# Kernel optimization log

Hardware: AMD Instinct MI355X
Metric: run time of the kernel (lower is better)

Reference implementation:

```python
import jax, jax.numpy as jnp
import numpy as np

N = 8192  # number of nodes


def _deg_norm(idx, n):
    # degree^{-1/2}, zero-degree clamped to 1 (DGL allow_zero_in_degree behavior)
    deg = jax.ops.segment_sum(jnp.ones(idx.shape[0], jnp.float32), idx, num_segments=n)
    return jax.lax.rsqrt(jnp.maximum(deg, 1.0))


def _graph_conv(h, src, dst, norm_src, norm_dst, W, b):
    # norm='both': scale at src, sparse sum-aggregate, scale at dst, then linear
    h = h * norm_src[:, None]
    m = jax.ops.segment_sum(h[src], dst, num_segments=h.shape[0])  # gather + scatter-add
    m = m * norm_dst[:, None]
    return m @ W + b


def setup_inputs() -> dict:
    key = jax.random.key(0)
    k = jax.random.split(key, 6)
    E = 262144
    x = jax.random.normal(k[0], (N, 256), jnp.float32)
    src = jax.random.randint(k[1], (E,), 0, N, jnp.int32)
    dst = jax.random.randint(k[2], (E,), 0, N, jnp.int32)
    W1 = jax.random.normal(k[3], (256, 128), jnp.float32) * (1.0 / np.sqrt(256))
    b1 = jnp.zeros((128,), jnp.float32)
    W2 = jax.random.normal(k[4], (128, 128), jnp.float32) * (1.0 / np.sqrt(128))
    b2 = jnp.zeros((128,), jnp.float32)
    return {"x": x, "src": src, "dst": dst, "W1": W1, "b1": b1, "W2": W2, "b2": b2}


def reference(x, src, dst, W1, b1, W2, b2):
    n = x.shape[0]
    norm_src = _deg_norm(src, n)  # out-degree norm
    norm_dst = _deg_norm(dst, n)  # in-degree norm
    # encode: GraphConv -> relu -> GraphConv  (dropout=0 -> identity)
    h = jax.nn.relu(_graph_conv(x, src, dst, norm_src, norm_dst, W1, b1))
    h = _graph_conv(h, src, dst, norm_src, norm_dst, W2, b2)
    # decode: sigmoid(h h^T), dense [N, N] reconstruction
    return jax.nn.sigmoid(h @ h.T)
```

## Files before the change

kernel.cpp:

```cpp
#include <hip/hip_runtime.h>
#include <hip/hip_bf16.h>

typedef __attribute__((ext_vector_type(8))) short short8;
typedef __attribute__((ext_vector_type(4))) float f32x4;

#define NNODES 8192
#define FDIM 128

__global__ void k_zero(int* __restrict__ p, int n) {
    int i = blockIdx.x * blockDim.x + threadIdx.x;
    if (i < n) p[i] = 0;
}

__global__ void k_deg_int(const int* __restrict__ src, const int* __restrict__ dst,
                          int* __restrict__ cnt_s, int* __restrict__ cnt_d, int E) {
    int e = blockIdx.x * blockDim.x + threadIdx.x;
    if (e < E) {
        atomicAdd(&cnt_s[src[e]], 1);
        atomicAdd(&cnt_d[dst[e]], 1);
    }
}

__global__ __launch_bounds__(256) void k_scan_norms(const int* __restrict__ cnt_s,
                                                    const int* __restrict__ cnt_d,
                                                    float* __restrict__ norm_s,
                                                    int* __restrict__ row_start,
                                                    int* __restrict__ cursor, int n) {
    __shared__ int partial[256];
    __shared__ int offs[257];
    int t = threadIdx.x;
    int base = t * 32;
#pragma unroll
    for (int i = 0; i < 32; ++i)
        norm_s[base + i] = rsqrtf(fmaxf((float)cnt_s[base + i], 1.0f));
    int local[32];
    int s = 0;
#pragma unroll
    for (int i = 0; i < 32; ++i) { local[i] = s; s += cnt_d[base + i]; }
    partial[t] = s;
    __syncthreads();
    if (t == 0) {
        int acc = 0;
        for (int i = 0; i < 256; ++i) { offs[i] = acc; acc += partial[i]; }
        offs[256] = acc;
    }
    __syncthreads();
    int o = offs[t];
#pragma unroll
    for (int i = 0; i < 32; ++i) {
        int v = o + local[i];
        row_start[base + i] = v;
        cursor[base + i] = v;
    }
    if (t == 0) row_start[n] = offs[256];
}

__global__ void k_fill(const int* __restrict__ src, const int* __restrict__ dst,
                       int* __restrict__ cursor, int* __restrict__ csr_src, int E) {
    int e = blockIdx.x * blockDim.x + threadIdx.x;
    if (e < E) {
        int pos = atomicAdd(&cursor[dst[e]], 1);
        csr_src[pos] = src[e];
    }
}

template<int K>
__global__ __launch_bounds__(256) void k_linear(const float* __restrict__ X,
                                                const float* __restrict__ W,
                                                const float* __restrict__ norm,
                                                float* __restrict__ Y) {
    __shared__ float xs[16][K];
    int t = threadIdx.x;
    int row0 = blockIdx.x * 16;
    constexpr int K4 = K / 4;
    constexpr int NCH = 16 * K4 / 256;
#pragma unroll
    for (int i = 0; i < NCH; ++i) {
        int c = t + i * 256;
        int r = c / K4, k4 = c % K4;
        *(float4*)&xs[r][k4 * 4] = *(const float4*)(X + (size_t)(row0 + r) * K + k4 * 4);
    }
    __syncthreads();

    int lane = t & 31, g = t >> 5;
    int r0 = g * 2, r1 = g * 2 + 1;
    int c = lane * 4;
    f32x4 acc0 = {0.f, 0.f, 0.f, 0.f}, acc1 = {0.f, 0.f, 0.f, 0.f};
    for (int k = 0; k < K; k += 4) {
        f32x4 x0 = *(f32x4*)&xs[r0][k];
        f32x4 x1 = *(f32x4*)&xs[r1][k];
#pragma unroll
        for (int kk = 0; kk < 4; ++kk) {
            f32x4 w = *(const f32x4*)(W + (size_t)(k + kk) * FDIM + c);
            acc0 += w * x0[kk];
            acc1 += w * x1[kk];
        }
    }
    float n0 = norm[row0 + r0], n1 = norm[row0 + r1];
    *(f32x4*)(Y + (size_t)(row0 + r0) * FDIM + c) = acc0 * n0;
    *(f32x4*)(Y + (size_t)(row0 + r1) * FDIM + c) = acc1 * n1;
}

static __device__ inline unsigned short f2bf(float f) {
    union { float f; unsigned int u; } a; a.f = f;
    unsigned int u = a.u;
    unsigned int r = u + 0x7FFFu + ((u >> 16) & 1u);
    return (unsigned short)(r >> 16);
}

template<int MODE>
__global__ __launch_bounds__(256) void k_gather_agg(const float* __restrict__ Y,
                                                    const int* __restrict__ row_start,
                                                    const int* __restrict__ csr_src,
                                                    const float* __restrict__ bias,
                                                    void* __restrict__ outp) {
    int t = threadIdx.x;
    int node = blockIdx.x * 8 + (t >> 5);
    int c4 = (t & 31) << 2;
    int beg = row_start[node], end = row_start[node + 1];
    f32x4 acc0 = {0.f, 0.f, 0.f, 0.f}, acc1 = {0.f, 0.f, 0.f, 0.f};
    int e = beg;
    for (; e + 3 < end; e += 4) {
        int s0 = csr_src[e], s1 = csr_src[e + 1], s2 = csr_src[e + 2], s3 = csr_src[e + 3];
        f32x4 v0 = *(const f32x4*)(Y + ((size_t)s0 << 7) + c4);
        f32x4 v1 = *(const f32x4*)(Y + ((size_t)s1 << 7) + c4);
        f32x4 v2 = *(const f32x4*)(Y + ((size_t)s2 << 7) + c4);
        f32x4 v3 = *(const f32x4*)(Y + ((size_t)s3 << 7) + c4);
        acc0 += v0; acc1 += v1; acc0 += v2; acc1 += v3;
    }
    for (; e < end; ++e) {
        int s0 = csr_src[e];
        acc0 += *(const f32x4*)(Y + ((size_t)s0 << 7) + c4);
    }
    f32x4 acc = acc0 + acc1;
    float scale = rsqrtf(fmaxf((float)(end - beg), 1.0f));
    f32x4 b = *(const f32x4*)(bias + c4);
    f32x4 v = acc * scale + b;
    if (MODE == 0) {
#pragma unroll
        for (int i = 0; i < 4; ++i) v[i] = fmaxf(v[i], 0.f);
        *(f32x4*)((float*)outp + ((size_t)node << 7) + c4) = v;
    } else {
        ushort4 u;
        u.x = f2bf(v[0]); u.y = f2bf(v[1]); u.z = f2bf(v[2]); u.w = f2bf(v[3]);
        *(ushort4*)((unsigned short*)outp + ((size_t)node << 7) + c4) = u;
    }
}

__global__ __launch_bounds__(256) void k_decode(const __hip_bfloat16* __restrict__ H,
                                                float* __restrict__ C) {
    const int ti = blockIdx.x, tj = blockIdx.y;
    if (tj < ti) return;
    __shared__ __align__(16) unsigned char smem[65536];
    unsigned char* sA = smem;
    unsigned char* sB = smem + 32768;
    const int t = threadIdx.x;
    const unsigned char* gH = (const unsigned char*)H;

#pragma unroll
    for (int i = 0; i < 8; ++i) {
        int chunk = t + i * 256;
        int row = chunk >> 4;
        int cc = (chunk & 15) << 4;
        int lofs = row * 256 + (cc ^ ((row & 7) << 4));
        *(float4*)(sA + lofs) = *(const float4*)(gH + ((size_t)(ti * 128 + row) << 8) + cc);
        *(float4*)(sB + lofs) = *(const float4*)(gH + ((size_t)(tj * 128 + row) << 8) + cc);
    }
    __syncthreads();

    const int w = t >> 6, lane = t & 63;
    const int wr = (w >> 1) * 64, wc = (w & 1) * 64;
    const int lr = lane & 15;
    const int lk = (lane >> 4) * 16;

    f32x4 acc[4][4] = {};

#pragma unroll
    for (int ks = 0; ks < 4; ++ks) {
        short8 af[4], bfr[4];
#pragma unroll
        for (int mi = 0; mi < 4; ++mi) {
            int row = wr + mi * 16 + lr;
            int off = row * 256 + ((ks * 64 + lk) ^ ((row & 7) << 4));
            af[mi] = *(const short8*)(sA + off);
        }
#pragma unroll
        for (int ni = 0; ni < 4; ++ni) {
            int row = wc + ni * 16 + lr;
            int off = row * 256 + ((ks * 64 + lk) ^ ((row & 7) << 4));
            bfr[ni] = *(const short8*)(sB + off);
        }
#pragma unroll
        for (int mi = 0; mi < 4; ++mi)
#pragma unroll
            for (int ni = 0; ni < 4; ++ni)
                acc[mi][ni] = __builtin_amdgcn_mfma_f32_16x16x32_bf16(af[mi], bfr[ni],
                                                                      acc[mi][ni], 0, 0, 0);
    }

    const int rbase = (lane >> 4) * 4;
    const int cbase = lane & 15;
#pragma unroll
    for (int mi = 0; mi < 4; ++mi) {
        int rowb = ti * 128 + wr + mi * 16 + rbase;
#pragma unroll
        for (int ni = 0; ni < 4; ++ni) {
            int col = tj * 128 + wc + ni * 16 + cbase;
            f32x4 s;
#pragma unroll
            for (int r = 0; r < 4; ++r)
                s[r] = 1.0f / (1.0f + __expf(-acc[mi][ni][r]));
            __builtin_nontemporal_store(s, (f32x4*)(C + (size_t)col * NNODES + rowb));
            if (ti != tj) {
#pragma unroll
                for (int r = 0; r < 4; ++r)
                    __builtin_nontemporal_store(s[r], C + (size_t)(rowb + r) * NNODES + col);
            }
        }
    }
}

extern "C" void kernel_launch(void* const* d_in, const int* in_sizes, int n_in,
                              void* d_out, int out_size, void* d_ws, size_t ws_size,
                              hipStream_t stream) {
    const float* x  = (const float*)d_in[0];
    const int* src  = (const int*)d_in[1];
    const int* dst  = (const int*)d_in[2];
    const float* W1 = (const float*)d_in[3];
    const float* b1 = (const float*)d_in[4];
    const float* W2 = (const float*)d_in[5];
    const float* b2 = (const float*)d_in[6];
    float* out = (float*)d_out;
    const int E = in_sizes[1];

    char* ws = (char*)d_ws;
    float* norm_s    = (float*)(ws + 0);
    int*   cnt_s     = (int*)(ws + (64 << 10));
    int*   cnt_d     = (int*)(ws + (96 << 10));
    int*   row_start = (int*)(ws + (128 << 10));
    int*   cursor    = (int*)(ws + (164 << 10));
    int*   csr_src   = (int*)(ws + (196 << 10));
    char*  big       = ws + (196 << 10) + ((size_t)E * 4);
    float* bufA      = (float*)big;
    float* bufB      = (float*)(big + (4 << 20));
    __hip_bfloat16* h2bf = (__hip_bfloat16*)(big + (8 << 20));

    k_zero<<<(2 * NNODES + 255) / 256, 256, 0, stream>>>(cnt_s, 2 * NNODES);

    k_deg_int<<<(E + 255) / 256, 256, 0, stream>>>(src, dst, cnt_s, cnt_d, E);
    k_scan_norms<<<1, 256, 0, stream>>>(cnt_s, cnt_d, norm_s, row_start, cursor, NNODES);
    k_fill<<<(E + 255) / 256, 256, 0, stream>>>(src, dst, cursor, csr_src, E);

    k_linear<256><<<NNODES / 16, 256, 0, stream>>>(x, W1, norm_s, bufA);
    k_gather_agg<0><<<NNODES / 8, 256, 0, stream>>>(bufA, row_start, csr_src, b1, bufB);

    k_linear<128><<<NNODES / 16, 256, 0, stream>>>(bufB, W2, norm_s, bufA);
    k_gather_agg<1><<<NNODES / 8, 256, 0, stream>>>(bufA, row_start, csr_src, b2, h2bf);

    k_decode<<<dim3(64, 64), 256, 0, stream>>>(h2bf, out);
}
```

Baseline: 211.9 us.

## Launch only upper-triangle decode tiles and transpose mirror tile through LDS

The decode grid now launches only the 2080 upper-triangular tile pairs, decoding each linear block index into (ti, tj) with a sqrt-based formula instead of launching 4096 blocks and returning early from half of them. The mirrored lower-triangle tile is staged transposed in shared memory with an XOR swizzle, then written back with coalesced 16-byte nontemporal row stores instead of scattered scalar stores. The direct tile also becomes scalar stores along rows. It adds two barriers, reuses the operand LDS, and holds all sigmoid values in registers, which may raise register pressure.

```diff
diff --git a/kernel.cpp b/kernel.cpp
--- a/kernel.cpp
+++ b/kernel.cpp
@@ -1,5 +1,6 @@
 #include <hip/hip_runtime.h>
 #include <hip/hip_bf16.h>
+#include <math.h>
 
 typedef __attribute__((ext_vector_type(8))) short short8;
 typedef __attribute__((ext_vector_type(4))) float f32x4;
@@ -149,8 +150,12 @@
 
 __global__ __launch_bounds__(256) void k_decode(const __hip_bfloat16* __restrict__ H,
                                                 float* __restrict__ C) {
-    const int ti = blockIdx.x, tj = blockIdx.y;
-    if (tj < ti) return;
+    int lin = blockIdx.x;
+    int ti = (int)((129.0 - sqrt(16641.0 - 8.0 * (double)lin)) * 0.5);
+    while (ti * (129 - ti) / 2 > lin) --ti;
+    while ((ti + 1) * (128 - ti) / 2 <= lin) ++ti;
+    int tj = ti + (lin - ti * (129 - ti) / 2);
+
     __shared__ __align__(16) unsigned char smem[65536];
     unsigned char* sA = smem;
     unsigned char* sB = smem + 32768;
@@ -200,23 +205,51 @@
 
     const int rbase = (lane >> 4) * 4;
     const int cbase = lane & 15;
+    f32x4 sv[4][4];
+#pragma unroll
+    for (int mi = 0; mi < 4; ++mi)
+#pragma unroll
+        for (int ni = 0; ni < 4; ++ni)
+#pragma unroll
+            for (int r = 0; r < 4; ++r)
+                sv[mi][ni][r] = 1.0f / (1.0f + __expf(-acc[mi][ni][r]));
+
 #pragma unroll
     for (int mi = 0; mi < 4; ++mi) {
         int rowb = ti * 128 + wr + mi * 16 + rbase;
 #pragma unroll
         for (int ni = 0; ni < 4; ++ni) {
             int col = tj * 128 + wc + ni * 16 + cbase;
-            f32x4 s;
 #pragma unroll
             for (int r = 0; r < 4; ++r)
-                s[r] = 1.0f / (1.0f + __expf(-acc[mi][ni][r]));
-            __builtin_nontemporal_store(s, (f32x4*)(C + (size_t)col * NNODES + rowb));
-            if (ti != tj) {
-#pragma unroll
-                for (int r = 0; r < 4; ++r)
-                    __builtin_nontemporal_store(s[r], C + (size_t)(rowb + r) * NNODES + col);
-            }
-        }
+                __builtin_nontemporal_store(sv[mi][ni][r], C + (size_t)(rowb + r) * NNODES + col);
+        }
+    }
+
+    if (ti == tj) return;
+
+    __syncthreads();
+    float* tileT = (float*)smem;
+#pragma unroll
+    for (int mi = 0; mi < 4; ++mi) {
+        int rowb = wr + mi * 16 + rbase;
+#pragma unroll
+        for (int ni = 0; ni < 4; ++ni) {
+            int col = wc + ni * 16 + cbase;
+            int off = col * 128 + (rowb ^ ((col & 15) << 2));
+            *(f32x4*)(tileT + off) = sv[mi][ni];
+        }
+    }
+    __syncthreads();
+
+#pragma unroll
+    for (int i = 0; i < 16; ++i) {
+        int chunk = i * 256 + t;
+        int mr = chunk >> 5;
+        int mc4 = (chunk & 31) << 2;
+        int off = mr * 128 + (mc4 ^ ((mr & 15) << 2));
+        f32x4 v = *(f32x4*)(tileT + off);
+        __builtin_nontemporal_store(v, (f32x4*)(C + (size_t)(tj * 128 + mr) * NNODES + ti * 128 + mc4));
     }
 }
 
@@ -257,5 +290,5 @@
     k_linear<128><<<NNODES / 16, 256, 0, stream>>>(bufB, W2, norm_s, bufA);
     k_gather_agg<1><<<NNODES / 8, 256, 0, stream>>>(bufA, row_start, csr_src, b2, h2bf);
 
-    k_decode<<<dim3(64, 64), 256, 0, stream>>>(h2bf, out);
-}
+    k_decode<<<64 * 65 / 2, 256, 0, stream>>>(h2bf, out);
+}
```

Measured after the change: 195.6 us. -7.7%, faster.
